# Performance work log

Hardware: AMD Instinct MI355X
Metric: run time of the kernel (lower is better)

The kernel has to match this reference:

```python
import jax, jax.numpy as jnp
import numpy as np

K = 3
DILATION = 1
DG = 1  # deformable groups


def _deform_conv2d(x, offsets, mask, weight, bias, k=K, dilation=DILATION, dg=DG):
    # x: [B, C, H, W]; offsets: [B, dg*2*k*k, H, W]; mask: [B, dg*k*k, H, W]
    # weight: [O, C, k, k]; bias: [O]
    B, C, H, W = x.shape
    O = weight.shape[0]
    Cg = C // dg
    kk = k * k
    pad = (k // 2) * dilation

    # base sampling grid per kernel tap (stride=1)
    ky, kx = jnp.meshgrid(jnp.arange(k), jnp.arange(k), indexing='ij')
    ky = ky.reshape(kk)
    kx = kx.reshape(kk)
    base_y = (jnp.arange(H)[None, :, None] - pad + ky[:, None, None] * dilation)  # [kk,H,1]
    base_x = (jnp.arange(W)[None, None, :] - pad + kx[:, None, None] * dilation)  # [kk,1,W]

    off = offsets.reshape(B, dg, kk, 2, H, W)
    py = base_y[None, None].astype(x.dtype) + off[:, :, :, 0]  # [B,dg,kk,H,W]
    px = base_x[None, None].astype(x.dtype) + off[:, :, :, 1]  # [B,dg,kk,H,W]

    y0 = jnp.floor(py)
    x0 = jnp.floor(px)
    wy1 = py - y0  # frac weights
    wx1 = px - x0
    wy0 = 1.0 - wy1
    wx0 = 1.0 - wx1

    img = x.reshape(B, dg, Cg, H * W)

    def gather(yi, xi):
        # yi, xi: float integer-valued coords [B,dg,kk,H,W]; zero outside bounds
        valid = (yi >= 0) & (yi <= H - 1) & (xi >= 0) & (xi <= W - 1)
        yc = jnp.clip(yi, 0, H - 1).astype(jnp.int32)
        xc = jnp.clip(xi, 0, W - 1).astype(jnp.int32)
        idx = (yc * W + xc).reshape(B, dg, 1, kk * H * W)
        vals = jnp.take_along_axis(img, idx, axis=3).reshape(B, dg, Cg, kk, H, W)
        return vals * valid.reshape(B, dg, 1, kk, H, W).astype(x.dtype)

    def w5(a):  # lift [B,dg,kk,H,W] -> [B,dg,1,kk,H,W]
        return a.reshape(B, dg, 1, kk, H, W)

    sampled = (gather(y0, x0) * w5(wy0 * wx0)
               + gather(y0, x0 + 1) * w5(wy0 * wx1)
               + gather(y0 + 1, x0) * w5(wy1 * wx0)
               + gather(y0 + 1, x0 + 1) * w5(wy1 * wx1))  # [B,dg,Cg,kk,H,W]

    sampled = sampled * mask.reshape(B, dg, 1, kk, H, W)
    sampled = sampled.reshape(B, C, kk, H, W)

    out = jnp.einsum('bckhw,ock->bohw', sampled, weight.reshape(O, C, kk))
    return out + bias[None, :, None, None]


def setup_inputs() -> dict:
    key = jax.random.key(0)
    k1, k2, k3, k4, k5 = jax.random.split(key, 5)
    B, C, O, H, W = 8, 128, 128, 64, 64
    x = jax.random.normal(k1, (B, C, H, W), dtype=jnp.float32)
    offsets = jax.random.normal(k2, (B, DG * 2 * K * K, H, W), dtype=jnp.float32)
    mask = jax.random.uniform(k3, (B, DG * K * K, H, W), dtype=jnp.float32)
    fan_in = C * K * K
    weight = jax.random.normal(k4, (O, C, K, K), dtype=jnp.float32) / np.sqrt(fan_in)
    bias = jax.random.normal(k5, (O,), dtype=jnp.float32) * 0.01
    return {"x": x, "offsets": offsets, "mask": mask, "weight": weight, "bias": bias}


def reference(x, offsets, mask, weight, bias):
    return _deform_conv2d(x, offsets, mask, weight, bias)
```

## Files before the change

### kernel.cpp

```cpp
#include <hip/hip_runtime.h>
#include <math.h>

constexpr int Bn = 8, Cn = 128, On = 128, Hn = 64, Wn = 64;
constexpr int KK = 9, PAD = 1;
constexpr int BDIM = 512;
constexpr int PXB  = 64;
constexpr int CG = 16, NG = Cn / CG;
constexpr int KG = 160, KTOT = NG * KG;
constexpr int BANDH = 11;
constexpr int RST  = 68;
constexpr int XSTP = 756;
constexpr int AST  = 84;
constexpr int ME   = KK * PXB;
constexpr int PB_DW  = 8 * XSTP;
constexpr int ASH_DW = PXB * AST;
constexpr int SM_DW  = PB_DW + 2 * ASH_DW;
constexpr int BUNITS = BANDH * 128;

typedef __attribute__((ext_vector_type(2))) _Float16 h2;
typedef __attribute__((ext_vector_type(8))) __fp16   f16x8;
typedef __attribute__((ext_vector_type(4))) float f32x4;
typedef unsigned short u16;
typedef unsigned int u32;

union UH  { u32 u; h2 h; };
union U4H { uint4 u; f16x8 h; };

__device__ __forceinline__ u32 pkh(float a, float b) {
    union { decltype(__builtin_amdgcn_cvt_pkrtz(0.f, 0.f)) p; u32 u; } t;
    t.p = __builtin_amdgcn_cvt_pkrtz(a, b);
    return t.u;
}
__device__ __forceinline__ h2 bch(u32 w) { UH t; t.u = w; return t.h; }
__device__ __forceinline__ u16 f2h(float f) {
    union { _Float16 h; u16 u; } v; v.h = (_Float16)f; return v.u;
}

__global__ void wprep_kernel(const float* __restrict__ w, u16* __restrict__ wh) {
    __shared__ u32 tmpw[KTOT / 2];
    u16* tmp = (u16*)tmpw;
    const int tid = threadIdx.x, o = blockIdx.x;
    if (tid < 64)
        tmpw[(tid >> 3) * 80 + 72 + (tid & 7)] = 0;
    for (int k = tid; k < Cn * KK; k += 256) {
        const int c = k / 9, t = k - 9 * c;
        tmp[(c >> 4) * KG + t * 16 + (c & 15)] = f2h(w[o * (Cn * KK) + k]);
    }
    __syncthreads();
    u32* dst = (u32*)(wh + (size_t)o * KTOT);
    for (int e = tid; e < KTOT / 2; e += 256) dst[e] = tmpw[e];
}

__device__ __forceinline__ void do_sample(const u32* __restrict__ pband,
                                          u32* __restrict__ ashW,
                                          const float* __restrict__ xg,
                                          const uint4 wp, const int2 q,
                                          const int2 ix, const int e)
{
    const int t = e >> 6, px = e & 63;
    u32 avp[8];
    if (!__any((q.x | q.y) < 0)) {
        const u32* p0 = pband + ix.x;
        const u32* p1 = pband + ix.y;
        const h2 w0 = bch(wp.x), w1 = bch(wp.y), w2 = bch(wp.z), w3 = bch(wp.w);
        #pragma unroll
        for (int c2 = 0; c2 < 8; ++c2) {
            const h2 vt0 = bch(p0[c2 * XSTP]), vt1 = bch(p0[c2 * XSTP + 1]);
            const h2 vb0 = bch(p1[c2 * XSTP]), vb1 = bch(p1[c2 * XSTP + 1]);
            const h2 r = w0 * vt0 + w1 * vt1 + w2 * vb0 + w3 * vb1;
            UH o; o.h = r; avp[c2] = o.u;
        }
    } else {
        const float fw0 = (float)bch(wp.x)[0], fw1 = (float)bch(wp.y)[0];
        const float fw2 = (float)bch(wp.z)[0], fw3 = (float)bch(wp.w)[0];
        const int qx = q.x < 0 ? ~q.x : q.x;
        const int qy = q.y < 0 ? ~q.y : q.y;
        const int yrx = qx >> 8, yry = qy >> 8;
        const int xx = (qx & 255) - 1, xy = (qy & 255) - 1;
        const int ax0 = max(xx, 0), ax1 = min(xx + 1, Wn - 1);
        const int ay0 = max(xy, 0), ay1 = min(xy + 1, Wn - 1);
        #pragma unroll
        for (int c2 = 0; c2 < 8; ++c2) {
            float v2[2];
            #pragma unroll
            for (int sb = 0; sb < 2; ++sb) {
                const float* gc = xg + ((2 * c2 + sb) << 12);
                const float t0 = gc[yrx * Wn + ax0], t1 = gc[yrx * Wn + ax1];
                const float b0 = gc[yry * Wn + ay0], b1 = gc[yry * Wn + ay1];
                v2[sb] = fmaf(fw0, t0, fmaf(fw1, t1, fmaf(fw2, b0, fw3 * b1)));
            }
            avp[c2] = pkh(v2[0], v2[1]);
        }
    }
    u32* d = ashW + px * AST + t * 8;
    *(uint4*)&d[0] = make_uint4(avp[0], avp[1], avp[2], avp[3]);
    *(uint4*)&d[4] = make_uint4(avp[4], avp[5], avp[6], avp[7]);
}

__global__ __launch_bounds__(BDIM, 4)
void dcn_mfma_kernel(const float* __restrict__ x,
                     const float* __restrict__ offs,
                     const float* __restrict__ mask,
                     const u16*   __restrict__ wh,
                     const float* __restrict__ bias,
                     float* __restrict__ out)
{
    __shared__ __align__(16) u32 smem[SM_DW];
    u32* const pband = smem;

    const int tid = threadIdx.x;
    const int b   = blockIdx.x & 7;
    const int h   = blockIdx.x >> 3;
    const int r0  = min(max(h - 5, 0), Hn - BANDH);

    const int s_px4 = tid & 15, s_pair = (tid >> 4) & 7;

    float4 bnda[3], bndb[3];
#define BLOAD(GCH) { \
        _Pragma("unroll") \
        for (int it = 0; it < 3; ++it) { \
            const int u = tid + it * BDIM; \
            if (u < BUNITS) { \
                const int row = u >> 7; \
                const float* bp = x + (((size_t)(b * Cn + (GCH) * CG + 2 * s_pair)) << 12) \
                                  + (r0 + row) * Wn + (s_px4 << 2); \
                bnda[it] = *(const float4*)bp; \
                bndb[it] = *(const float4*)(bp + 4096); \
            } \
        } }
#define BWRITE() { \
        _Pragma("unroll") \
        for (int it = 0; it < 3; ++it) { \
            const int u = tid + it * BDIM; \
            if (u < BUNITS) { \
                const int row = u >> 7; \
                u32* d = &pband[s_pair * XSTP + row * RST + 8 + (s_px4 << 2)]; \
                *(uint4*)d = make_uint4( \
                    pkh(bnda[it].x, bndb[it].x), pkh(bnda[it].y, bndb[it].y), \
                    pkh(bnda[it].z, bndb[it].z), pkh(bnda[it].w, bndb[it].w)); \
            } \
        } }

    BLOAD(0);

    uint4 mwp[2]; int2 mq[2]; int2 mi[2];
    #pragma unroll
    for (int it = 0; it < 2; ++it) {
        mwp[it] = make_uint4(0, 0, 0, 0);
        mq[it] = make_int2(r0 << 8, r0 << 8);
        mi[it] = make_int2(7, 7);
        const int e = tid + it * BDIM;
        if (e < ME) {
            const int t = e >> 6, px = e & 63;
            const int ty = t / 3, tx = t - ty * 3;
            const float oy = offs[((b * 18 + 2 * t    ) * Hn + h) * Wn + px];
            const float ox = offs[((b * 18 + 2 * t + 1) * Hn + h) * Wn + px];
            const float m  = mask[((b * KK + t) * Hn + h) * Wn + px];
            const float py = (float)(h - PAD + ty) + oy;
            const float qx = (float)(px - PAD + tx) + ox;
            const float fy = floorf(py), fx = floorf(qx);
            const float wy1 = py - fy, wx1 = qx - fx;
            const float wy0 = 1.f - wy1, wx0 = 1.f - wx1;
            const int y0 = (int)fy, x0 = (int)fx;
            const bool cx0 = (x0 >= 0) && (x0 < Wn);
            const bool cx1 = (x0 >= -1) && (x0 < Wn - 1);
            const float wr[2] = { wy0, wy1 };
            float wout[4]; int qout[2], iout[2];
            #pragma unroll
            for (int j = 0; j < 2; ++j) {
                const int yr = y0 + j;
                const bool rv = (yr >= 0) && (yr < Hn);
                wout[2 * j]     = (rv && cx0) ? wr[j] * wx0 * m : 0.f;
                wout[2 * j + 1] = (rv && cx1) ? wr[j] * wx1 * m : 0.f;
                int qv;
                if (!rv || (!cx0 && !cx1)) qv = r0 << 8;
                else                       qv = (yr << 8) | (x0 + 1);
                const bool inband = (qv >> 8) >= r0 && (qv >> 8) < r0 + BANDH;
                qout[j] = inband ? qv : ~qv;
                iout[j] = ((qv >> 8) - r0) * RST + (qv & 255) + 7;
            }
            mwp[it] = make_uint4(pkh(wout[0], wout[0]), pkh(wout[1], wout[1]),
                                 pkh(wout[2], wout[2]), pkh(wout[3], wout[3]));
            mq[it] = make_int2(qout[0], qout[1]);
            mi[it] = make_int2(iout[0], iout[1]);
        }
    }

    if (tid < 416) {
        const int pair = tid / 52, j = tid - pair * 52;
        const int off = (j < 8) ? j : RST * ((j - 8) >> 2) + 72 + ((j - 8) & 3);
        pband[pair * XSTP + off] = 0;
    }
    #pragma unroll
    for (int it = 0; it < 2; ++it) {
        const int u = tid + it * BDIM;
        smem[PB_DW + (u >> 9) * ASH_DW + ((u & 511) >> 3) * AST + 72 + (u & 7)] = 0;
    }

    BWRITE();
    BLOAD(1);
    __syncthreads();

    const int wv = tid >> 6, ln = tid & 63, quad = ln >> 4, l16 = ln & 15;
    const int mrow = wv >> 1, ncol = wv & 1;
    const u16* wrow0 = wh + (size_t)(mrow * 32 + l16) * KTOT;
    const int npx0 = ncol * 32 + l16, npx1 = npx0 + 16;

    {
        const float* xg = x + (((size_t)(b * Cn)) << 12);
        do_sample(pband, smem + PB_DW, xg, mwp[0], mq[0], mi[0], tid);
        if (tid < 64)
            do_sample(pband, smem + PB_DW, xg, mwp[1], mq[1], mi[1], BDIM + tid);
    }
    __syncthreads();

    f32x4 acc[2][2];
    #pragma unroll
    for (int mt = 0; mt < 2; ++mt)
        #pragma unroll
        for (int nt = 0; nt < 2; ++nt) acc[mt][nt] = (f32x4){0.f, 0.f, 0.f, 0.f};

    f16x8 pa0[2], pa1[2];
#define APRE(GG) { const int kgp = (GG) * KG + quad * 8; \
        pa0[0] = *(const f16x8*)(wrow0 + kgp); \
        pa1[0] = *(const f16x8*)(wrow0 + 16 * KTOT + kgp); \
        pa0[1] = *(const f16x8*)(wrow0 + kgp + 32); \
        pa1[1] = *(const f16x8*)(wrow0 + 16 * KTOT + kgp + 32); }
    APRE(0);

#define MSTEP_PRE(S) { \
        const int kd = (S) * 16 + quad * 4; \
        U4H b0, b1; \
        b0.u = *(const uint4*)&ad[npx0 * AST + kd]; \
        b1.u = *(const uint4*)&ad[npx1 * AST + kd]; \
        acc[0][0] = __builtin_amdgcn_mfma_f32_16x16x32_f16(pa0[S], b0.h, acc[0][0], 0, 0, 0); \
        acc[0][1] = __builtin_amdgcn_mfma_f32_16x16x32_f16(pa0[S], b1.h, acc[0][1], 0, 0, 0); \
        acc[1][0] = __builtin_amdgcn_mfma_f32_16x16x32_f16(pa1[S], b0.h, acc[1][0], 0, 0, 0); \
        acc[1][1] = __builtin_amdgcn_mfma_f32_16x16x32_f16(pa1[S], b1.h, acc[1][1], 0, 0, 0); }

#define MSTEP_LD(S) { \
        const int kg = g * KG + (S) * 32 + quad * 8; \
        const f16x8 a0 = *(const f16x8*)(wrow0 + kg); \
        const f16x8 a1 = *(const f16x8*)(wrow0 + 16 * KTOT + kg); \
        const int kd = (S) * 16 + quad * 4; \
        U4H b0, b1; \
        b0.u = *(const uint4*)&ad[npx0 * AST + kd]; \
        b1.u = *(const uint4*)&ad[npx1 * AST + kd]; \
        acc[0][0] = __builtin_amdgcn_mfma_f32_16x16x32_f16(a0, b0.h, acc[0][0], 0, 0, 0); \
        acc[0][1] = __builtin_amdgcn_mfma_f32_16x16x32_f16(a0, b1.h, acc[0][1], 0, 0, 0); \
        acc[1][0] = __builtin_amdgcn_mfma_f32_16x16x32_f16(a1, b0.h, acc[1][0], 0, 0, 0); \
        acc[1][1] = __builtin_amdgcn_mfma_f32_16x16x32_f16(a1, b1.h, acc[1][1], 0, 0, 0); }

    for (int g = 0; g < NG; ++g) {
        const u32* ad = smem + PB_DW + (g & 1) * ASH_DW;
        u32* ashN     = smem + PB_DW + ((g + 1) & 1) * ASH_DW;
        if (g + 1 < NG) BWRITE();
        MSTEP_PRE(0);
        MSTEP_PRE(1);
        __syncthreads();
        if (g + 2 < NG) BLOAD(g + 2);
        if (g + 1 < NG) {
            const float* xg = x + (((size_t)(b * Cn + (g + 1) * CG)) << 12);
            do_sample(pband, ashN, xg, mwp[0], mq[0], mi[0], tid);
            if (tid < 64)
                do_sample(pband, ashN, xg, mwp[1], mq[1], mi[1], BDIM + tid);
        }
        MSTEP_LD(2);
        MSTEP_LD(3);
        MSTEP_LD(4);
        if (g + 1 < NG) APRE(g + 1);
        __syncthreads();
    }

    float* tr = (float*)smem;
    #pragma unroll
    for (int mt = 0; mt < 2; ++mt)
        #pragma unroll
        for (int nt = 0; nt < 2; ++nt)
            #pragma unroll
            for (int r = 0; r < 4; ++r) {
                const int o  = mrow * 32 + mt * 16 + quad * 4 + r;
                const int px = ncol * 32 + nt * 16 + l16;
                tr[o * 68 + px] = acc[mt][nt][r] + bias[o];
            }
    __syncthreads();
    {
        const int orow = tid >> 2, f0 = tid & 3;
        #pragma unroll
        for (int it = 0; it < 4; ++it) {
            const int f = f0 + it * 4;
            const float4 v = *(const float4*)&tr[orow * 68 + (f << 2)];
            *(float4*)&out[(((size_t)b * On + orow) * Hn + h) * Wn + (f << 2)] = v;
        }
    }
#undef BLOAD
#undef BWRITE
#undef APRE
#undef MSTEP_PRE
#undef MSTEP_LD
}

constexpr int FBD = 256;
constexpr int FB_PXB = 32, FB_CCH = 4, FB_NCT = FB_CCH * KK, FB_MW = KK * FB_PXB;

#define FMA4(A, S, W)                          \
    A.x = fmaf((S).x, (W), A.x);               \
    A.y = fmaf((S).y, (W), A.y);               \
    A.z = fmaf((S).z, (W), A.z);               \
    A.w = fmaf((S).w, (W), A.w);

__global__ __launch_bounds__(FBD, 4)
void dcn_fb_kernel(const float* __restrict__ x,
                   const float* __restrict__ offs,
                   const float* __restrict__ mask,
                   const float* __restrict__ weight,
                   const float* __restrict__ bias,
                   float* __restrict__ out)
{
    __shared__ float wmeta[4 * FB_MW];
    __shared__ int   imeta[4 * FB_MW];
    __shared__ float ssh[FB_NCT * FB_PXB];
    __shared__ float wsh[FB_NCT * On];

    const int tid    = threadIdx.x;
    const int b      = blockIdx.x & 7;
    const int rem    = blockIdx.x >> 3;
    const int h      = rem >> 1;
    const int pxbase = (rem & 1) * FB_PXB;

    for (int e = tid; e < FB_MW; e += FBD) {
        const int t  = e >> 5;
        const int px = e & 31;
        const int pg = pxbase + px;
        const int ty = t / 3, tx = t - ty * 3;
        const float oy = offs[((b * 18 + 2 * t    ) * Hn + h) * Wn + pg];
        const float ox = offs[((b * 18 + 2 * t + 1) * Hn + h) * Wn + pg];
        const float m  = mask[((b * KK + t) * Hn + h) * Wn + pg];
        const float py = (float)(h - PAD + ty) + oy;
        const float qx = (float)(pg - PAD + tx) + ox;
        const float y0 = floorf(py), x0 = floorf(qx);
        const float wy1 = py - y0, wx1 = qx - x0;
        const float wy0 = 1.f - wy1, wx0 = 1.f - wx1;
        const float cw[4] = { wy0 * wx0, wy0 * wx1, wy1 * wx0, wy1 * wx1 };
        #pragma unroll
        for (int k = 0; k < 4; ++k) {
            const float yk = y0 + (float)(k >> 1);
            const float xk = x0 + (float)(k & 1);
            const bool valid = (yk >= 0.f) && (yk <= (float)(Hn - 1)) &&
                               (xk >= 0.f) && (xk <= (float)(Wn - 1));
            const int yc = (int)fminf(fmaxf(yk, 0.f), (float)(Hn - 1));
            const int xc = (int)fminf(fmaxf(xk, 0.f), (float)(Wn - 1));
            wmeta[k * FB_MW + e] = valid ? cw[k] * m : 0.f;
            imeta[k * FB_MW + e] = yc * Wn + xc;
        }
    }
    __syncthreads();

    const int px0 = (tid & 7) << 2;
    const int oo  = (tid >> 3) << 2;

    float4 acc[4];
    #pragma unroll
    for (int j = 0; j < 4; ++j) acc[j] = make_float4(0.f, 0.f, 0.f, 0.f);

    for (int cb = 0; cb < Cn / FB_CCH; ++cb) {
        #pragma unroll
        for (int it = 0; it < (FB_NCT * On) / FBD; ++it) {
            const int e = tid + it * FBD;
            const int r = e >> 7;
            const int o = e & 127;
            wsh[r * On + o] = weight[o * (Cn * KK) + cb * FB_NCT + r];
        }
        for (int e = tid; e < FB_NCT * FB_PXB; e += FBD) {
            const int px = e & 31;
            const int ct = e >> 5;
            const int c  = ct / 9;
            const int mb = (ct - c * 9) * FB_PXB + px;
            const float* xp = x + (((b * Cn) + cb * FB_CCH + c) << 12);
            float v =  wmeta[mb]              * xp[imeta[mb]];
            v = fmaf(wmeta[FB_MW     + mb], xp[imeta[FB_MW     + mb]], v);
            v = fmaf(wmeta[2 * FB_MW + mb], xp[imeta[2 * FB_MW + mb]], v);
            v = fmaf(wmeta[3 * FB_MW + mb], xp[imeta[3 * FB_MW + mb]], v);
            ssh[ct * FB_PXB + px] = v;
        }
        __syncthreads();

        #pragma unroll 6
        for (int ct = 0; ct < FB_NCT; ++ct) {
            const float4 sv = *(const float4*)&ssh[ct * FB_PXB + px0];
            const float4 wa = *(const float4*)&wsh[ct * On + oo];
            FMA4(acc[0], sv, wa.x);
            FMA4(acc[1], sv, wa.y);
            FMA4(acc[2], sv, wa.z);
            FMA4(acc[3], sv, wa.w);
        }
        __syncthreads();
    }

    #pragma unroll
    for (int j = 0; j < 4; ++j) {
        const float bv = bias[oo + j];
        float4 r = acc[j];
        r.x += bv; r.y += bv; r.z += bv; r.w += bv;
        *(float4*)&out[((b * On + oo + j) * Hn + h) * Wn + pxbase + px0] = r;
    }
}

extern "C" void kernel_launch(void* const* d_in, const int* in_sizes, int n_in,
                              void* d_out, int out_size, void* d_ws, size_t ws_size,
                              hipStream_t stream) {
    const float* x      = (const float*)d_in[0];
    const float* offs   = (const float*)d_in[1];
    const float* mask   = (const float*)d_in[2];
    const float* weight = (const float*)d_in[3];
    const float* bias   = (const float*)d_in[4];
    float* out = (float*)d_out;

    const size_t need = (size_t)On * KTOT * sizeof(u16);
    if (d_ws != nullptr && ws_size >= need) {
        u16* wh = (u16*)d_ws;
        wprep_kernel<<<dim3(On), dim3(256), 0, stream>>>(weight, wh);
        dcn_mfma_kernel<<<dim3(Bn * Hn), dim3(BDIM), 0, stream>>>(
            x, offs, mask, wh, bias, out);
    } else {
        dcn_fb_kernel<<<dim3(Bn * Hn * 2), dim3(FBD), 0, stream>>>(
            x, offs, mask, weight, bias, out);
    }
}
```

Measured before the change: 138.9 us.

## Split fused deformable conv into im2col kernel plus separate MFMA GEMM kernel

Replaces the single fused sample-and-MFMA kernel with two kernels when workspace is large enough. The first kernel writes the bilinearly sampled, masked fp16 columns to a global buffer, parallelized over batch, row and channel-group halves. The second kernel runs the MFMA GEMM directly from global memory and stages the output through shared memory so the stores are coalesced. This decouples sampling from the matrix multiply to gain parallelism and occupancy, at the cost of writing and re-reading roughly 84 MB of intermediate data through HBM.

After: 188.2 us. +35.5%, slower.

```diff
diff --git a/kernel.cpp b/kernel.cpp
--- a/kernel.cpp
+++ b/kernel.cpp
@@ -17,6 +17,11 @@
 constexpr int SM_DW  = PB_DW + 2 * ASH_DW;
 constexpr int BUNITS = BANDH * 128;
 
+constexpr int    KRD     = 640;
+constexpr size_t S_DW    = (size_t)Bn * 4096 * KRD;
+constexpr size_t S_BYTES = S_DW * 4;
+constexpr size_t WH_BYTES = (size_t)On * KTOT * 2;
+
 typedef __attribute__((ext_vector_type(2))) _Float16 h2;
 typedef __attribute__((ext_vector_type(8))) __fp16   f16x8;
 typedef __attribute__((ext_vector_type(4))) float f32x4;
@@ -51,14 +56,11 @@
     for (int e = tid; e < KTOT / 2; e += 256) dst[e] = tmpw[e];
 }
 
-__device__ __forceinline__ void do_sample(const u32* __restrict__ pband,
-                                          u32* __restrict__ ashW,
-                                          const float* __restrict__ xg,
-                                          const uint4 wp, const int2 q,
-                                          const int2 ix, const int e)
+__device__ __forceinline__ void sample_core(const u32* __restrict__ pband,
+                                            const float* __restrict__ xg,
+                                            const uint4 wp, const int2 q,
+                                            const int2 ix, u32* avp)
 {
-    const int t = e >> 6, px = e & 63;
-    u32 avp[8];
     if (!__any((q.x | q.y) < 0)) {
         const u32* p0 = pband + ix.x;
         const u32* p1 = pband + ix.y;
@@ -92,28 +94,52 @@
             avp[c2] = pkh(v2[0], v2[1]);
         }
     }
+}
+
+__device__ __forceinline__ void do_sample(const u32* __restrict__ pband,
+                                          u32* __restrict__ ashW,
+                                          const float* __restrict__ xg,
+                                          const uint4 wp, const int2 q,
+                                          const int2 ix, const int e)
+{
+    const int t = e >> 6, px = e & 63;
+    u32 avp[8];
+    sample_core(pband, xg, wp, q, ix, avp);
     u32* d = ashW + px * AST + t * 8;
     *(uint4*)&d[0] = make_uint4(avp[0], avp[1], avp[2], avp[3]);
     *(uint4*)&d[4] = make_uint4(avp[4], avp[5], avp[6], avp[7]);
 }
 
+__device__ __forceinline__ void do_sample_g(const u32* __restrict__ pband,
+                                            u32* __restrict__ Sg,
+                                            const float* __restrict__ xg,
+                                            const uint4 wp, const int2 q,
+                                            const int2 ix, const int e,
+                                            const int g)
+{
+    const int t = e >> 6, px = e & 63;
+    u32 avp[8];
+    sample_core(pband, xg, wp, q, ix, avp);
+    u32* d = Sg + (size_t)px * KRD + g * 80 + t * 8;
+    *(uint4*)&d[0] = make_uint4(avp[0], avp[1], avp[2], avp[3]);
+    *(uint4*)&d[4] = make_uint4(avp[4], avp[5], avp[6], avp[7]);
+}
+
 __global__ __launch_bounds__(BDIM, 4)
-void dcn_mfma_kernel(const float* __restrict__ x,
-                     const float* __restrict__ offs,
-                     const float* __restrict__ mask,
-                     const u16*   __restrict__ wh,
-                     const float* __restrict__ bias,
-                     float* __restrict__ out)
+void dcn_im2col(const float* __restrict__ x,
+                const float* __restrict__ offs,
+                const float* __restrict__ mask,
+                u32* __restrict__ S32)
 {
-    __shared__ __align__(16) u32 smem[SM_DW];
-    u32* const pband = smem;
-
-    const int tid = threadIdx.x;
-    const int b   = blockIdx.x & 7;
-    const int h   = blockIdx.x >> 3;
-    const int r0  = min(max(h - 5, 0), Hn - BANDH);
-
+    __shared__ __align__(16) u32 pband[PB_DW];
+
+    const int tid  = threadIdx.x;
+    const int b    = blockIdx.x & 7;
+    const int h    = (blockIdx.x >> 3) & 63;
+    const int g0   = (blockIdx.x >> 9) * 4;
+    const int r0   = min(max(h - 5, 0), Hn - BANDH);
     const int s_px4 = tid & 15, s_pair = (tid >> 4) & 7;
+    u32* const Sg = S32 + ((size_t)b * 4096 + h * 64) * KRD;
 
     float4 bnda[3], bndb[3];
 #define BLOAD(GCH) { \
@@ -141,7 +167,7 @@
             } \
         } }
 
-    BLOAD(0);
+    BLOAD(g0);
 
     uint4 mwp[2]; int2 mq[2]; int2 mi[2];
     #pragma unroll
@@ -192,6 +218,199 @@
         pband[pair * XSTP + off] = 0;
     }
     #pragma unroll
+    for (int it = 0; it < 4; ++it) {
+        const int u = tid + it * BDIM;
+        const int px = u >> 5, gg = (u >> 3) & 3, j = u & 7;
+        Sg[(size_t)px * KRD + (g0 + gg) * 80 + 72 + j] = 0;
+    }
+
+    BWRITE();
+    BLOAD(g0 + 1);
+    __syncthreads();
+
+    const float* xb = x + (((size_t)(b * Cn)) << 12);
+    for (int gg = 0; gg < 4; ++gg) {
+        const int g = g0 + gg;
+        const float* xg = xb + (((size_t)(g * CG)) << 12);
+        do_sample_g(pband, Sg, xg, mwp[0], mq[0], mi[0], tid, g);
+        if (tid < 64)
+            do_sample_g(pband, Sg, xg, mwp[1], mq[1], mi[1], BDIM + tid, g);
+        if (gg < 3) {
+            __syncthreads();
+            BWRITE();
+            if (gg < 2) BLOAD(g0 + gg + 2);
+            __syncthreads();
+        }
+    }
+#undef BLOAD
+#undef BWRITE
+}
+
+__global__ __launch_bounds__(BDIM, 4)
+void dcn_gemm(const u32* __restrict__ S32,
+              const u16* __restrict__ wh,
+              const float* __restrict__ bias,
+              float* __restrict__ out)
+{
+    __shared__ __align__(16) float tr[128 * 68];
+
+    const int tid = threadIdx.x;
+    const int b   = blockIdx.x & 7;
+    const int h   = blockIdx.x >> 3;
+
+    const int wv = tid >> 6, ln = tid & 63, quad = ln >> 4, l16 = ln & 15;
+    const int mrow = wv >> 1, ncol = wv & 1;
+    const u16* wrow0 = wh + (size_t)(mrow * 32 + l16) * KTOT;
+    const int npx0 = ncol * 32 + l16, npx1 = npx0 + 16;
+    const u32* Srow = S32 + ((size_t)b * 4096 + h * 64) * KRD;
+    const u32* r0p = Srow + (size_t)npx0 * KRD;
+    const u32* r1p = Srow + (size_t)npx1 * KRD;
+
+    f32x4 acc[2][2];
+    #pragma unroll
+    for (int mt = 0; mt < 2; ++mt)
+        #pragma unroll
+        for (int nt = 0; nt < 2; ++nt) acc[mt][nt] = (f32x4){0.f, 0.f, 0.f, 0.f};
+
+    #pragma unroll 1
+    for (int g = 0; g < NG; ++g) {
+        f16x8 pa[5][2];
+        const int kgp = g * KG + quad * 8;
+        #pragma unroll
+        for (int s = 0; s < 5; ++s) {
+            pa[s][0] = *(const f16x8*)(wrow0 + kgp + s * 32);
+            pa[s][1] = *(const f16x8*)(wrow0 + 16 * KTOT + kgp + s * 32);
+        }
+        const int kb = g * 80 + quad * 4;
+        #pragma unroll
+        for (int s = 0; s < 5; ++s) {
+            U4H b0, b1;
+            b0.u = *(const uint4*)&r0p[kb + s * 16];
+            b1.u = *(const uint4*)&r1p[kb + s * 16];
+            acc[0][0] = __builtin_amdgcn_mfma_f32_16x16x32_f16(pa[s][0], b0.h, acc[0][0], 0, 0, 0);
+            acc[0][1] = __builtin_amdgcn_mfma_f32_16x16x32_f16(pa[s][0], b1.h, acc[0][1], 0, 0, 0);
+            acc[1][0] = __builtin_amdgcn_mfma_f32_16x16x32_f16(pa[s][1], b0.h, acc[1][0], 0, 0, 0);
+            acc[1][1] = __builtin_amdgcn_mfma_f32_16x16x32_f16(pa[s][1], b1.h, acc[1][1], 0, 0, 0);
+        }
+    }
+
+    #pragma unroll
+    for (int mt = 0; mt < 2; ++mt)
+        #pragma unroll
+        for (int nt = 0; nt < 2; ++nt)
+            #pragma unroll
+            for (int r = 0; r < 4; ++r) {
+                const int o  = mrow * 32 + mt * 16 + quad * 4 + r;
+                const int px = ncol * 32 + nt * 16 + l16;
+                tr[o * 68 + px] = acc[mt][nt][r] + bias[o];
+            }
+    __syncthreads();
+    {
+        const int orow = tid >> 2, f0 = tid & 3;
+        #pragma unroll
+        for (int it = 0; it < 4; ++it) {
+            const int f = f0 + it * 4;
+            const float4 v = *(const float4*)&tr[orow * 68 + (f << 2)];
+            *(float4*)&out[(((size_t)b * On + orow) * Hn + h) * Wn + (f << 2)] = v;
+        }
+    }
+}
+
+__global__ __launch_bounds__(BDIM, 4)
+void dcn_mfma_kernel(const float* __restrict__ x,
+                     const float* __restrict__ offs,
+                     const float* __restrict__ mask,
+                     const u16*   __restrict__ wh,
+                     const float* __restrict__ bias,
+                     float* __restrict__ out)
+{
+    __shared__ __align__(16) u32 smem[SM_DW];
+    u32* const pband = smem;
+
+    const int tid = threadIdx.x;
+    const int b   = blockIdx.x & 7;
+    const int h   = blockIdx.x >> 3;
+    const int r0  = min(max(h - 5, 0), Hn - BANDH);
+
+    const int s_px4 = tid & 15, s_pair = (tid >> 4) & 7;
+
+    float4 bnda[3], bndb[3];
+#define BLOAD(GCH) { \
+        _Pragma("unroll") \
+        for (int it = 0; it < 3; ++it) { \
+            const int u = tid + it * BDIM; \
+            if (u < BUNITS) { \
+                const int row = u >> 7; \
+                const float* bp = x + (((size_t)(b * Cn + (GCH) * CG + 2 * s_pair)) << 12) \
+                                  + (r0 + row) * Wn + (s_px4 << 2); \
+                bnda[it] = *(const float4*)bp; \
+                bndb[it] = *(const float4*)(bp + 4096); \
+            } \
+        } }
+#define BWRITE() { \
+        _Pragma("unroll") \
+        for (int it = 0; it < 3; ++it) { \
+            const int u = tid + it * BDIM; \
+            if (u < BUNITS) { \
+                const int row = u >> 7; \
+                u32* d = &pband[s_pair * XSTP + row * RST + 8 + (s_px4 << 2)]; \
+                *(uint4*)d = make_uint4( \
+                    pkh(bnda[it].x, bndb[it].x), pkh(bnda[it].y, bndb[it].y), \
+                    pkh(bnda[it].z, bndb[it].z), pkh(bnda[it].w, bndb[it].w)); \
+            } \
+        } }
+
+    BLOAD(0);
+
+    uint4 mwp[2]; int2 mq[2]; int2 mi[2];
+    #pragma unroll
+    for (int it = 0; it < 2; ++it) {
+        mwp[it] = make_uint4(0, 0, 0, 0);
+        mq[it] = make_int2(r0 << 8, r0 << 8);
+        mi[it] = make_int2(7, 7);
+        const int e = tid + it * BDIM;
+        if (e < ME) {
+            const int t = e >> 6, px = e & 63;
+            const int ty = t / 3, tx = t - ty * 3;
+            const float oy = offs[((b * 18 + 2 * t    ) * Hn + h) * Wn + px];
+            const float ox = offs[((b * 18 + 2 * t + 1) * Hn + h) * Wn + px];
+            const float m  = mask[((b * KK + t) * Hn + h) * Wn + px];
+            const float py = (float)(h - PAD + ty) + oy;
+            const float qx = (float)(px - PAD + tx) + ox;
+            const float fy = floorf(py), fx = floorf(qx);
+            const float wy1 = py - fy, wx1 = qx - fx;
+            const float wy0 = 1.f - wy1, wx0 = 1.f - wx1;
+            const int y0 = (int)fy, x0 = (int)fx;
+            const bool cx0 = (x0 >= 0) && (x0 < Wn);
+            const bool cx1 = (x0 >= -1) && (x0 < Wn - 1);
+            const float wr[2] = { wy0, wy1 };
+            float wout[4]; int qout[2], iout[2];
+            #pragma unroll
+            for (int j = 0; j < 2; ++j) {
+                const int yr = y0 + j;
+                const bool rv = (yr >= 0) && (yr < Hn);
+                wout[2 * j]     = (rv && cx0) ? wr[j] * wx0 * m : 0.f;
+                wout[2 * j + 1] = (rv && cx1) ? wr[j] * wx1 * m : 0.f;
+                int qv;
+                if (!rv || (!cx0 && !cx1)) qv = r0 << 8;
+                else                       qv = (yr << 8) | (x0 + 1);
+                const bool inband = (qv >> 8) >= r0 && (qv >> 8) < r0 + BANDH;
+                qout[j] = inband ? qv : ~qv;
+                iout[j] = ((qv >> 8) - r0) * RST + (qv & 255) + 7;
+            }
+            mwp[it] = make_uint4(pkh(wout[0], wout[0]), pkh(wout[1], wout[1]),
+                                 pkh(wout[2], wout[2]), pkh(wout[3], wout[3]));
+            mq[it] = make_int2(qout[0], qout[1]);
+            mi[it] = make_int2(iout[0], iout[1]);
+        }
+    }
+
+    if (tid < 416) {
+        const int pair = tid / 52, j = tid - pair * 52;
+        const int off = (j < 8) ? j : RST * ((j - 8) >> 2) + 72 + ((j - 8) & 3);
+        pband[pair * XSTP + off] = 0;
+    }
+    #pragma unroll
     for (int it = 0; it < 2; ++it) {
         const int u = tid + it * BDIM;
         smem[PB_DW + (u >> 9) * ASH_DW + ((u & 511) >> 3) * AST + 72 + (u & 7)] = 0;
@@ -416,8 +635,15 @@
     const float* bias   = (const float*)d_in[4];
     float* out = (float*)d_out;
 
-    const size_t need = (size_t)On * KTOT * sizeof(u16);
-    if (d_ws != nullptr && ws_size >= need) {
+    const size_t need_fused = WH_BYTES;
+    const size_t need_split = S_BYTES + WH_BYTES;
+    if (d_ws != nullptr && ws_size >= need_split) {
+        u32* S32 = (u32*)d_ws;
+        u16* wh  = (u16*)((char*)d_ws + S_BYTES);
+        wprep_kernel<<<dim3(On), dim3(256), 0, stream>>>(weight, wh);
+        dcn_im2col<<<dim3(2 * Bn * Hn), dim3(BDIM), 0, stream>>>(x, offs, mask, S32);
+        dcn_gemm<<<dim3(Bn * Hn), dim3(BDIM), 0, stream>>>(S32, wh, bias, out);
+    } else if (d_ws != nullptr && ws_size >= need_fused) {
         u16* wh = (u16*)d_ws;
         wprep_kernel<<<dim3(On), dim3(256), 0, stream>>>(weight, wh);
         dcn_mfma_kernel<<<dim3(Bn * Hn), dim3(BDIM), 0, stream>>>(
```
